# Performance work log

Hardware: AMD Instinct MI355X
Metric: run time of the kernel (lower is better)

The kernel has to match this reference:

```python
import jax, jax.numpy as jnp
import numpy as np

B, T, C, H = 4, 4096, 1024, 128

def setup_inputs() -> dict:
    key = jax.random.key(0)
    k1, k2, k3, k4 = jax.random.split(key, 4)
    x = jax.random.normal(k1, (B, T, C), dtype=jnp.float32)
    # nn.Linear(embed, head, bias=False): y = x @ W, store W as [C, H]
    s = 1.0 / np.sqrt(C)
    Wk = jax.random.normal(k2, (C, H), dtype=jnp.float32) * s
    Wq = jax.random.normal(k3, (C, H), dtype=jnp.float32) * s
    Wv = jax.random.normal(k4, (C, H), dtype=jnp.float32) * s
    return {"x": x, "Wk": Wk, "Wq": Wq, "Wv": Wv}

def reference(x, Wk, Wq, Wv):
    Bx, Tx, Cx = x.shape
    scale = Wk.shape[1] ** -0.5
    k = x @ Wk  # [B,T,H]
    q = x @ Wq
    v = x @ Wv
    att = jnp.einsum('bth,bsh->bts', q, k) * scale  # [B,T,T]
    causal = jnp.triu(jnp.ones((Tx, Tx), dtype=bool), k=1)
    att = jnp.where(causal, -jnp.inf, att)
    att = jax.nn.softmax(att, axis=-1)
    # dropout is identity in eval mode
    out = jnp.einsum('bts,bsh->bth', att, v)  # [B,T,H]
    return out
```

## Files before the change

kernel.cpp:

```cpp
#include <hip/hip_runtime.h>
#include <stdint.h>
#include <math.h>

#define B_ 4
#define T_ 4096
#define C_ 1024
#define H_ 128

typedef __attribute__((ext_vector_type(8))) short s16x8;
typedef __attribute__((ext_vector_type(4))) float f32x4;

__device__ __forceinline__ unsigned short f2bf(float f) {
    union { float f; unsigned u; } v; v.f = f;
    unsigned r = v.u + 0x7fffu + ((v.u >> 16) & 1u);
    return (unsigned short)(r >> 16);
}

__device__ __forceinline__ s16x8 as_frag(uint4 u) {
    union { uint4 u; s16x8 s; } v; v.u = u; return v.s;
}

__host__ __device__ constexpr int chunks_total(int CH) {
    int a = 64 / CH, b = 64 % CH;
    return CH * a * (a + 1) / 2 + b * (a + 1);
}

#define QSC (0.0883883476f * 1.4426950408f)

__global__ __launch_bounds__(256) void k_wt(const float* __restrict__ Wk,
                                            const float* __restrict__ Wq,
                                            const float* __restrict__ Wv,
                                            unsigned short* __restrict__ Wt) {
    __shared__ float tile[64][65];
    int w = blockIdx.z;
    const float* W = (w == 0) ? Wk : (w == 1) ? Wq : Wv;
    int c0 = blockIdx.x * 64, h0 = blockIdx.y * 64;
    int tid = threadIdx.x;
#pragma unroll
    for (int k = 0; k < 16; k++) {
        int idx = tid + k * 256;
        int r = idx >> 6, c = idx & 63;
        tile[r][c] = W[(size_t)(c0 + r) * H_ + h0 + c];
    }
    __syncthreads();
#pragma unroll
    for (int k = 0; k < 16; k++) {
        int idx = tid + k * 256;
        int hh = idx >> 6, cc = idx & 63;
        Wt[(size_t)(w * H_ + h0 + hh) * C_ + c0 + cc] = f2bf(tile[cc][hh]);
    }
}

__global__ __launch_bounds__(256, 3) void k_qkv(const float* __restrict__ x,
                                                const unsigned short* __restrict__ Wt,
                                                unsigned short* __restrict__ Qb,
                                                unsigned short* __restrict__ Kb,
                                                unsigned short* __restrict__ Vt) {
    __shared__ unsigned short a_lds[2][64 * 72];
    int tid = threadIdx.x;
    int wv = tid >> 6, lane = tid & 63, quad = lane >> 4, lo = lane & 15;
    int r0 = blockIdx.x * 64;
    int cb = blockIdx.y;
    int nt0 = wv * 3;

    f32x4 acc[3][4];
#pragma unroll
    for (int i = 0; i < 3; i++)
#pragma unroll
        for (int j = 0; j < 4; j++) acc[i][j] = (f32x4){0.f, 0.f, 0.f, 0.f};

    const int row_s = tid >> 2;
    const int seg_s = (tid & 3) * 16;
    size_t xbase = (size_t)(r0 + row_s) * C_ + seg_s;

    const unsigned short* wp[3];
#pragma unroll
    for (int nt = 0; nt < 3; nt++)
        wp[nt] = Wt + (size_t)(cb * 192 + (nt0 + nt) * 16 + lo) * C_ + quad * 8;

    auto pack_store = [&](unsigned short* buf, const float4 (&f)[4]) {
        uint4 u0, u1;
        u0.x = (unsigned)f2bf(f[0].x) | ((unsigned)f2bf(f[0].y) << 16);
        u0.y = (unsigned)f2bf(f[0].z) | ((unsigned)f2bf(f[0].w) << 16);
        u0.z = (unsigned)f2bf(f[1].x) | ((unsigned)f2bf(f[1].y) << 16);
        u0.w = (unsigned)f2bf(f[1].z) | ((unsigned)f2bf(f[1].w) << 16);
        u1.x = (unsigned)f2bf(f[2].x) | ((unsigned)f2bf(f[2].y) << 16);
        u1.y = (unsigned)f2bf(f[2].z) | ((unsigned)f2bf(f[2].w) << 16);
        u1.z = (unsigned)f2bf(f[3].x) | ((unsigned)f2bf(f[3].y) << 16);
        u1.w = (unsigned)f2bf(f[3].z) | ((unsigned)f2bf(f[3].w) << 16);
        *(uint4*)&buf[row_s * 72 + seg_s] = u0;
        *(uint4*)&buf[row_s * 72 + seg_s + 8] = u1;
    };
    auto load_x = [&](float4 (&f)[4], int kc) {
        const float* xp = x + xbase + kc * 64;
#pragma unroll
        for (int j = 0; j < 4; j++) f[j] = *(const float4*)(xp + j * 4);
    };
    auto compute = [&](const unsigned short* buf, int kc) {
        s16x8 b[3][2];
#pragma unroll
        for (int nt = 0; nt < 3; nt++)
#pragma unroll
            for (int kh = 0; kh < 2; kh++)
                b[nt][kh] = *(const s16x8*)(wp[nt] + kc * 64 + kh * 32);
        s16x8 af[4][2];
#pragma unroll
        for (int mt = 0; mt < 4; mt++)
#pragma unroll
            for (int kh = 0; kh < 2; kh++)
                af[mt][kh] = *(const s16x8*)&buf[(mt * 16 + lo) * 72 + kh * 32 + quad * 8];
#pragma unroll
        for (int nt = 0; nt < 3; nt++)
#pragma unroll
            for (int kh = 0; kh < 2; kh++)
#pragma unroll
                for (int mt = 0; mt < 4; mt++)
                    acc[nt][mt] = __builtin_amdgcn_mfma_f32_16x16x32_bf16(
                        af[mt][kh], b[nt][kh], acc[nt][mt], 0, 0, 0);
    };

    float4 x0[4], x1[4];
    load_x(x0, 0);
    load_x(x1, 1);
    pack_store(a_lds[0], x0);
    __syncthreads();

    for (int kc2 = 0; kc2 < 8; kc2++) {
        int kc = kc2 * 2;
        if (kc + 2 < 16) load_x(x0, kc + 2);
        compute(a_lds[0], kc);
        pack_store(a_lds[1], x1);
        __syncthreads();
        if (kc + 3 < 16) load_x(x1, kc + 3);
        compute(a_lds[1], kc + 1);
        if (kc + 2 < 16) pack_store(a_lds[0], x0);
        __syncthreads();
    }

#pragma unroll
    for (int nt = 0; nt < 3; nt++) {
        int col = cb * 192 + (nt0 + nt) * 16 + lo;
        int w = col >> 7, h = col & 127;
#pragma unroll
        for (int mt = 0; mt < 4; mt++) {
            int mrow = r0 + mt * 16 + quad * 4;
            if (w == 2) {
                int b = mrow >> 12, t0 = mrow & 4095;
                int tp = (t0 & ~31) + (((t0 & 15) >> 2) << 3) + (((t0 >> 4) & 1) << 2);
                uint2 pk;
                pk.x = (unsigned)f2bf(acc[nt][mt][0]) | ((unsigned)f2bf(acc[nt][mt][1]) << 16);
                pk.y = (unsigned)f2bf(acc[nt][mt][2]) | ((unsigned)f2bf(acc[nt][mt][3]) << 16);
                *(uint2*)(Vt + (size_t)(b * H_ + h) * T_ + tp) = pk;
            } else if (w == 1) {
                unsigned short* dst = Qb + (size_t)mrow * H_ + h;
#pragma unroll
                for (int r = 0; r < 4; r++)
                    dst[(size_t)r * H_] = f2bf(acc[nt][mt][r] * QSC);
            } else {
                unsigned short* dst = Kb + (size_t)mrow * H_ + h;
#pragma unroll
                for (int r = 0; r < 4; r++)
                    dst[(size_t)r * H_] = f2bf(acc[nt][mt][r]);
            }
        }
    }
}

#define LOAD_KV(kv0)                                                            \
    do {                                                                        \
        const uint4* kg = (const uint4*)(Kb + (size_t)(batch * T_ + (kv0) + srow_k) * H_); \
        pk0 = kg[sseg_k + 0]; pk1 = kg[sseg_k + 1];                             \
        pk2 = kg[sseg_k + 2]; pk3 = kg[sseg_k + 3];                             \
        const uint4* vg = (const uint4*)(Vt + (size_t)(batch * H_ + srow_v) * T_ + (kv0)); \
        pv0 = vg[sseg_v + 0]; pv1 = vg[sseg_v + 1];                             \
        pv2 = vg[sseg_v + 2]; pv3 = vg[sseg_v + 3];                             \
    } while (0)

template <int CH>
__global__ __launch_bounds__(256, 4) void k_attn(const unsigned short* __restrict__ Qb,
                                                 const unsigned short* __restrict__ Kb,
                                                 const unsigned short* __restrict__ Vt,
                                                 float* __restrict__ Opart,
                                                 float* __restrict__ Mpart,
                                                 float* __restrict__ Lpart,
                                                 float* __restrict__ out) {
    __shared__ uint4 kbuf[64 * 16];
    __shared__ uint4 vbuf[128 * 8];

    int tid = threadIdx.x;
    int wv = tid >> 6, lane = tid & 63, quad = lane >> 4, lo = lane & 15;

    int id = blockIdx.x;
    int qt, batch, tbeg, tend, slot = 0;
    if constexpr (CH > 0) {
        slot = id >> 2; batch = id & 3;
        int s = slot, q = 63;
        for (;;) { int nc = (q + CH) / CH; if (s < nc) break; s -= nc; --q; }
        qt = q;
        tbeg = s * CH;
        tend = min(tbeg + CH, qt + 1);
    } else {
        qt = 63 - (id >> 2); batch = id & 3;
        tbeg = 0; tend = qt + 1;
    }
    int m0 = qt * 64 + wv * 16;
    int query = m0 + lo;

    s16x8 qf[4];
    size_t qrow = (size_t)(batch * T_ + m0 + lo) * H_;
#pragma unroll
    for (int ks = 0; ks < 4; ks++)
        qf[ks] = *(const s16x8*)(Qb + qrow + ks * 32 + quad * 8);

    f32x4 acc_o[8];
#pragma unroll
    for (int o = 0; o < 8; o++) acc_o[o] = (f32x4){0.f, 0.f, 0.f, 0.f};
    float m_i = -INFINITY, l_i = 0.f;

    const int srow_k = tid >> 2, sseg_k = (tid & 3) * 4;
    const int srow_v = tid >> 1, sseg_v = (tid & 1) * 4;

    uint4 pk0, pk1, pk2, pk3, pv0, pv1, pv2, pv3;
    LOAD_KV(tbeg * 64);

    for (int t = tbeg; t < tend; ++t) {
        int kv0 = t * 64;
        kbuf[srow_k * 16 + ((sseg_k + 0) ^ (srow_k & 15))] = pk0;
        kbuf[srow_k * 16 + ((sseg_k + 1) ^ (srow_k & 15))] = pk1;
        kbuf[srow_k * 16 + ((sseg_k + 2) ^ (srow_k & 15))] = pk2;
        kbuf[srow_k * 16 + ((sseg_k + 3) ^ (srow_k & 15))] = pk3;
        vbuf[srow_v * 8 + ((sseg_v + 0) ^ (srow_v & 7))] = pv0;
        vbuf[srow_v * 8 + ((sseg_v + 1) ^ (srow_v & 7))] = pv1;
        vbuf[srow_v * 8 + ((sseg_v + 2) ^ (srow_v & 7))] = pv2;
        vbuf[srow_v * 8 + ((sseg_v + 3) ^ (srow_v & 7))] = pv3;
        __syncthreads();
        if (t + 1 < tend) LOAD_KV((t + 1) * 64);

        f32x4 s_acc[4];
#pragma unroll
        for (int nt = 0; nt < 4; nt++) s_acc[nt] = (f32x4){0.f, 0.f, 0.f, 0.f};
        __builtin_amdgcn_s_setprio(1);
#pragma unroll
        for (int ks = 0; ks < 4; ks++) {
#pragma unroll
            for (int nt = 0; nt < 4; nt++) {
                s16x8 kf = as_frag(kbuf[(nt * 16 + lo) * 16 + ((ks * 4 + quad) ^ lo)]);
                s_acc[nt] = __builtin_amdgcn_mfma_f32_16x16x32_bf16(kf, qf[ks], s_acc[nt], 0, 0, 0);
            }
        }
        __builtin_amdgcn_s_setprio(0);

        float p[4][4];
#pragma unroll
        for (int nt = 0; nt < 4; nt++)
#pragma unroll
            for (int r = 0; r < 4; r++) p[nt][r] = s_acc[nt][r];
        if (t == qt) {
#pragma unroll
            for (int nt = 0; nt < 4; nt++)
#pragma unroll
                for (int r = 0; r < 4; r++)
                    if (kv0 + nt * 16 + quad * 4 + r > query) p[nt][r] = -INFINITY;
        }

        float mx = p[0][0];
#pragma unroll
        for (int nt = 0; nt < 4; nt++)
#pragma unroll
            for (int r = 0; r < 4; r++) mx = fmaxf(mx, p[nt][r]);
        if (__any(mx > m_i + 8.0f)) {
            float rm = fmaxf(mx, __shfl_xor(mx, 16));
            rm = fmaxf(rm, __shfl_xor(rm, 32));
            float mnew = fmaxf(m_i, rm);
            float alpha = exp2f(m_i - mnew);
            l_i *= alpha;
            m_i = mnew;
#pragma unroll
            for (int o = 0; o < 8; o++)
#pragma unroll
                for (int r = 0; r < 4; r++) acc_o[o][r] *= alpha;
        }
        float rs = 0.f;
#pragma unroll
        for (int nt = 0; nt < 4; nt++)
#pragma unroll
            for (int r = 0; r < 4; r++) {
                float pv = exp2f(p[nt][r] - m_i);
                p[nt][r] = pv;
                rs += pv;
            }
        l_i += rs;

        s16x8 pf[2];
#pragma unroll
        for (int kt = 0; kt < 2; kt++) {
            uint4 u;
            u.x = (__float_as_uint(p[2 * kt][0]) >> 16) | ((__float_as_uint(p[2 * kt][1]) >> 16) << 16);
            u.y = (__float_as_uint(p[2 * kt][2]) >> 16) | ((__float_as_uint(p[2 * kt][3]) >> 16) << 16);
            u.z = (__float_as_uint(p[2 * kt + 1][0]) >> 16) | ((__float_as_uint(p[2 * kt + 1][1]) >> 16) << 16);
            u.w = (__float_as_uint(p[2 * kt + 1][2]) >> 16) | ((__float_as_uint(p[2 * kt + 1][3]) >> 16) << 16);
            pf[kt] = as_frag(u);
        }

        __builtin_amdgcn_s_setprio(1);
#pragma unroll
        for (int kt = 0; kt < 2; kt++)
#pragma unroll
            for (int o = 0; o < 8; o++) {
                int vrow = o * 16 + lo;
                s16x8 vf = as_frag(vbuf[vrow * 8 + ((kt * 4 + quad) ^ (vrow & 7))]);
                acc_o[o] = __builtin_amdgcn_mfma_f32_16x16x32_bf16(vf, pf[kt], acc_o[o], 0, 0, 0);
            }
        __builtin_amdgcn_s_setprio(0);
        __syncthreads();
    }

    l_i += __shfl_xor(l_i, 16);
    l_i += __shfl_xor(l_i, 32);

    if constexpr (CH > 0) {
        constexpr int NCH = chunks_total(CH);
        size_t pr = (size_t)(batch * NCH + slot) * 64 + wv * 16 + lo;
        float* Op = Opart + pr * 128;
#pragma unroll
        for (int o = 0; o < 8; o++) {
            float4 v = {acc_o[o][0], acc_o[o][1], acc_o[o][2], acc_o[o][3]};
            *(float4*)(Op + o * 16 + quad * 4) = v;
        }
        if (quad == 0) { Mpart[pr] = m_i; Lpart[pr] = l_i; }
    } else {
        float inv = 1.0f / l_i;
        int rowg = batch * T_ + m0 + lo;
#pragma unroll
        for (int o = 0; o < 8; o++) {
            float4 v = {acc_o[o][0] * inv, acc_o[o][1] * inv,
                        acc_o[o][2] * inv, acc_o[o][3] * inv};
            *(float4*)(out + (size_t)rowg * H_ + o * 16 + quad * 4) = v;
        }
    }
}

template <int CH>
__global__ __launch_bounds__(256) void k_comb(const float* __restrict__ Opart,
                                              const float* __restrict__ Mpart,
                                              const float* __restrict__ Lpart,
                                              float* __restrict__ out) {
    constexpr int NCH = chunks_total(CH);
    int tid = threadIdx.x;
    int row = blockIdx.x * 8 + (tid >> 5);
    int h4 = (tid & 31) * 4;
    int batch = row >> 12, t = row & 4095, qt = t >> 6;
    int n = qt + 1;
    int nc = (qt + CH) / CH;
    int a = n / CH, b = n % CH;
    int S = CH * a * (a + 1) / 2 + b * (a + 1);
    int base = NCH - S;
    float M = -INFINITY, den = 0.f;
    float4 o = {0.f, 0.f, 0.f, 0.f};
    for (int s = 0; s < nc; ++s) {
        size_t pr = (size_t)(batch * NCH + base + s) * 64 + (t & 63);
        float ms = Mpart[pr], ls = Lpart[pr];
        float4 v = *(const float4*)(Opart + pr * 128 + h4);
        float Mn = fmaxf(M, ms);
        float wa = exp2f(M - Mn), wb = exp2f(ms - Mn);
        den = den * wa + ls * wb;
        o.x = o.x * wa + v.x * wb;
        o.y = o.y * wa + v.y * wb;
        o.z = o.z * wa + v.z * wb;
        o.w = o.w * wa + v.w * wb;
        M = Mn;
    }
    float inv = 1.0f / den;
    float4 r = {o.x * inv, o.y * inv, o.z * inv, o.w * inv};
    *(float4*)(out + (size_t)row * H_ + h4) = r;
}

extern "C" void kernel_launch(void* const* d_in, const int* in_sizes, int n_in,
                              void* d_out, int out_size, void* d_ws, size_t ws_size,
                              hipStream_t stream) {
    const float* x  = (const float*)d_in[0];
    const float* Wk = (const float*)d_in[1];
    const float* Wq = (const float*)d_in[2];
    const float* Wv = (const float*)d_in[3];
    char* ws = (char*)d_ws;
    unsigned short* Wt = (unsigned short*)ws;
    unsigned short* Qb = (unsigned short*)(ws + (1u << 20));
    unsigned short* Kb = (unsigned short*)(ws + (5u << 20));
    unsigned short* Vt = (unsigned short*)(ws + (9u << 20));
    float* out = (float*)d_out;

    const size_t base = (size_t)13 << 20;
    constexpr int NCH10 = chunks_total(10);
    constexpr int NCH21 = chunks_total(21);
    auto need_for = [&](int nch) {
        return base + (size_t)4 * nch * 64 * (128 * 4) + 2 * (size_t)4 * nch * 64 * 4;
    };

    k_wt  <<<dim3(16, 2, 3), 256, 0, stream>>>(Wk, Wq, Wv, Wt);
    k_qkv <<<dim3(256, 2), 256, 0, stream>>>(x, Wt, Qb, Kb, Vt);

    if (ws_size >= need_for(NCH10)) {
        float* Op = (float*)(ws + base);
        float* Mp = Op + (size_t)4 * NCH10 * 64 * 128;
        float* Lp = Mp + (size_t)4 * NCH10 * 64;
        k_attn<10><<<4 * NCH10, 256, 0, stream>>>(Qb, Kb, Vt, Op, Mp, Lp, out);
        k_comb<10><<<2048, 256, 0, stream>>>(Op, Mp, Lp, out);
    } else if (ws_size >= need_for(NCH21)) {
        float* Op = (float*)(ws + base);
        float* Mp = Op + (size_t)4 * NCH21 * 64 * 128;
        float* Lp = Mp + (size_t)4 * NCH21 * 64;
        k_attn<21><<<4 * NCH21, 256, 0, stream>>>(Qb, Kb, Vt, Op, Mp, Lp, out);
        k_comb<21><<<2048, 256, 0, stream>>>(Op, Mp, Lp, out);
    } else {
        k_attn<0><<<256, 256, 0, stream>>>(Qb, Kb, Vt, nullptr, nullptr, nullptr, out);
    }
}
```

Baseline: 174.6 us.

## Simplify QKV pipeline, remap attention block ids, use nontemporal output stores

The QKV projection loop drops the manually unrolled two-stage register buffering in favour of a single loop that prefetches the next x chunk into registers while computing on the current LDS buffer. The attention kernel changes how block ids map to (slot, batch) so that adjacent chunk slots interleave across batches, meant to spread work across XCDs and improve cache locality. Partial and final output stores become nontemporal to avoid polluting caches. The simpler loop may expose more load latency per iteration, and the remap needs an even chunk count, which is checked with a static assert.

```diff
diff --git a/kernel.cpp b/kernel.cpp
--- a/kernel.cpp
+++ b/kernel.cpp
@@ -96,7 +96,16 @@
 #pragma unroll
         for (int j = 0; j < 4; j++) f[j] = *(const float4*)(xp + j * 4);
     };
-    auto compute = [&](const unsigned short* buf, int kc) {
+
+    float4 xr[4];
+    load_x(xr, 0);
+    pack_store(a_lds[0], xr);
+    __syncthreads();
+
+    for (int kc = 0; kc < 16; kc++) {
+        const unsigned short* buf = a_lds[kc & 1];
+        float4 xn[4];
+        if (kc < 15) load_x(xn, kc + 1);
         s16x8 b[3][2];
 #pragma unroll
         for (int nt = 0; nt < 3; nt++)
@@ -117,23 +126,7 @@
                 for (int mt = 0; mt < 4; mt++)
                     acc[nt][mt] = __builtin_amdgcn_mfma_f32_16x16x32_bf16(
                         af[mt][kh], b[nt][kh], acc[nt][mt], 0, 0, 0);
-    };
-
-    float4 x0[4], x1[4];
-    load_x(x0, 0);
-    load_x(x1, 1);
-    pack_store(a_lds[0], x0);
-    __syncthreads();
-
-    for (int kc2 = 0; kc2 < 8; kc2++) {
-        int kc = kc2 * 2;
-        if (kc + 2 < 16) load_x(x0, kc + 2);
-        compute(a_lds[0], kc);
-        pack_store(a_lds[1], x1);
-        __syncthreads();
-        if (kc + 3 < 16) load_x(x1, kc + 3);
-        compute(a_lds[1], kc + 1);
-        if (kc + 2 < 16) pack_store(a_lds[0], x0);
+        if (kc < 15) pack_store((unsigned short*)a_lds[(kc & 1) ^ 1], xn);
         __syncthreads();
     }
 
@@ -193,7 +186,10 @@
     int id = blockIdx.x;
     int qt, batch, tbeg, tend, slot = 0;
     if constexpr (CH > 0) {
-        slot = id >> 2; batch = id & 3;
+        int e = id & 1;
+        batch = (id >> 1) & 3;
+        int g = id >> 3;
+        slot = g * 2 + e;
         int s = slot, q = 63;
         for (;;) { int nc = (q + CH) / CH; if (s < nc) break; s -= nc; --q; }
         qt = q;
@@ -323,19 +319,17 @@
         size_t pr = (size_t)(batch * NCH + slot) * 64 + wv * 16 + lo;
         float* Op = Opart + pr * 128;
 #pragma unroll
-        for (int o = 0; o < 8; o++) {
-            float4 v = {acc_o[o][0], acc_o[o][1], acc_o[o][2], acc_o[o][3]};
-            *(float4*)(Op + o * 16 + quad * 4) = v;
-        }
+        for (int o = 0; o < 8; o++)
+            __builtin_nontemporal_store(acc_o[o], (f32x4*)(Op + o * 16 + quad * 4));
         if (quad == 0) { Mpart[pr] = m_i; Lpart[pr] = l_i; }
     } else {
         float inv = 1.0f / l_i;
         int rowg = batch * T_ + m0 + lo;
 #pragma unroll
         for (int o = 0; o < 8; o++) {
-            float4 v = {acc_o[o][0] * inv, acc_o[o][1] * inv,
-                        acc_o[o][2] * inv, acc_o[o][3] * inv};
-            *(float4*)(out + (size_t)rowg * H_ + o * 16 + quad * 4) = v;
+            f32x4 v = {acc_o[o][0] * inv, acc_o[o][1] * inv,
+                       acc_o[o][2] * inv, acc_o[o][3] * inv};
+            __builtin_nontemporal_store(v, (f32x4*)(out + (size_t)rowg * H_ + o * 16 + quad * 4));
         }
     }
 }
@@ -392,6 +386,7 @@
     const size_t base = (size_t)13 << 20;
     constexpr int NCH10 = chunks_total(10);
     constexpr int NCH21 = chunks_total(21);
+    static_assert(NCH10 % 2 == 0 && NCH21 % 2 == 0, "XCD decode needs even NCH");
     auto need_for = [&](int nch) {
         return base + (size_t)4 * nch * 64 * (128 * 4) + 2 * (size_t)4 * nch * 64 * 4;
     };
```

Result: no change. 173.0 us (-0.9%).
